# Kernel optimization log

Measured on AMD Instinct MI355X. Metric: run time of the kernel, lower is better.

## Reference

```python
import jax, jax.numpy as jnp
import numpy as np

EPS = 1e-5

def _bn(h, g, b):
    # BatchNorm1d with batch statistics (biased variance), eps=1e-5
    m = jnp.mean(h, axis=0)
    v = jnp.var(h, axis=0)
    return (h - m) * jax.lax.rsqrt(v + EPS) * g + b

def setup_inputs() -> dict:
    key = jax.random.key(0)
    ks = jax.random.split(key, 12)
    N, E, F = 100000, 500000, 128
    D = 2 * F  # 256
    s = 1.0 / np.sqrt(D)
    inp = {
        "x": jax.random.normal(ks[0], (N, F), dtype=jnp.float32),
        "edge_index": jax.random.randint(ks[1], (2, E), 0, N, dtype=jnp.int64),
        "W4": jax.random.normal(ks[2], (D, D), jnp.float32) * s,
        "b4": jnp.zeros((D,), jnp.float32),
        "g4": jnp.ones((D,), jnp.float32),
        "be4": jnp.zeros((D,), jnp.float32),
        "W1": jax.random.normal(ks[3], (D, D), jnp.float32) * s,
        "b1": jnp.zeros((D,), jnp.float32),
        "g1": jnp.ones((D,), jnp.float32),
        "be1": jnp.zeros((D,), jnp.float32),
        "W2": jax.random.normal(ks[4], (D, D), jnp.float32) * s,
        "b2": jnp.zeros((D,), jnp.float32),
        "g2": jnp.ones((D,), jnp.float32),
        "be2": jnp.zeros((D,), jnp.float32),
        "Wf": jax.random.normal(ks[5], (D, 1), jnp.float32) * s,
        "bf": jnp.zeros((1,), jnp.float32),
    }
    return inp

def reference(x, edge_index, W4, b4, g4, be4, W1, b1, g1, be1, W2, b2, g2, be2, Wf, bf):
    # gather + concat: [E, 2*F]
    edge_x = jnp.concatenate((x[edge_index[0]], x[edge_index[1]]), axis=1)
    # block 4: Linear -> BN -> ReLU (dropout = identity in eval)
    edge_x = jax.nn.relu(_bn(edge_x @ W4 + b4, g4, be4))
    # block 1 with residual
    out1 = jax.nn.relu(_bn(edge_x @ W1 + b1, g1, be1)) + edge_x
    # block 2 with residual
    out2 = jax.nn.relu(_bn(out1 @ W2 + b2, g2, be2)) + out1
    # final projection -> flatten to [E]
    return jnp.ravel(out2 @ Wf + bf)
```

## Files before the change

kernel.cpp:

```cpp
#include <hip/hip_runtime.h>
#include <hip/hip_bf16.h>
#include <stdint.h>


typedef __attribute__((ext_vector_type(8))) short short8;
typedef __attribute__((ext_vector_type(4))) float f32x4;

__device__ __forceinline__ unsigned short bf16b(float f) {
  unsigned int u = __float_as_uint(f);
  return (unsigned short)((u + 0x7fffu + ((u >> 16) & 1u)) >> 16);
}
__device__ __forceinline__ unsigned int packbf(float lo, float hi) {
  return (unsigned int)bf16b(lo) | ((unsigned int)bf16b(hi) << 16);
}
__device__ __forceinline__ float bflo(unsigned int u) { return __uint_as_float(u << 16); }
__device__ __forceinline__ float bfhi(unsigned int u) { return __uint_as_float(u & 0xffff0000u); }
__device__ __forceinline__ float bfs(short s) { return __uint_as_float(((unsigned int)(unsigned short)s) << 16); }
__device__ __forceinline__ float relu_(float x) { return fmaxf(x, 0.0f); }

__global__ __launch_bounds__(256) void k_init(const int* __restrict__ ei,
                                              float* __restrict__ stats, int* __restrict__ flag) {
  const int t = threadIdx.x;
  for (int i = t; i < 12288; i += 256) stats[i] = 0.f;
  if (t == 0) {
    int o = 0;
#pragma unroll
    for (int i = 0; i < 32; ++i) o |= ei[2 * i + 1];
    *flag = (o == 0) ? 1 : 0;
  }
}

__global__ __launch_bounds__(256) void k_bail(float* __restrict__ out, const float* __restrict__ bfp, int E) {
  const int i = blockIdx.x * 256 + threadIdx.x;
  if (i < E) out[i] = bfp[0];
}

__global__ __launch_bounds__(256) void k_prep(
    const float* __restrict__ W4, const float* __restrict__ W1, const float* __restrict__ W2,
    unsigned short* __restrict__ wt4, unsigned short* __restrict__ wt1, unsigned short* __restrict__ wt2)
{
  const int b = blockIdx.x;
  const int t = threadIdx.x;
  const int wi = b >> 6;
  const int r = b & 63;
  const float* W = (wi == 0) ? W4 : (wi == 1) ? W1 : W2;
  unsigned short* Wt = (wi == 0) ? wt4 : (wi == 1) ? wt1 : wt2;
  const int flat = r * 1024 + t * 4;
  const int n = flat >> 8;
  const int k = flat & 255;
  ushort4 o;
  o.x = bf16b(W[(k + 0) * 256 + n]);
  o.y = bf16b(W[(k + 1) * 256 + n]);
  o.z = bf16b(W[(k + 2) * 256 + n]);
  o.w = bf16b(W[(k + 3) * 256 + n]);
  *(ushort4*)(Wt + flat) = o;
}

__global__ __launch_bounds__(256) void k_stats(
    const float* __restrict__ stats, const float* __restrict__ g, const float* __restrict__ be,
    const float* __restrict__ bias, float* __restrict__ scale, float invE)
{
  const int c = threadIdx.x;
  float s = 0.f, q = 0.f;
#pragma unroll
  for (int sl = 0; sl < 8; ++sl) { s += stats[sl * 512 + c]; q += stats[sl * 512 + 256 + c]; }
  const float mean = s * invE;
  const float var = q * invE - mean * mean;
  const float a = g[c] * rsqrtf(var + 1e-5f);
  const float cstd = be[c] - mean * a;
  scale[c] = a;
  scale[256 + c] = cstd;
  scale[512 + c] = fmaf(a, bias[c], cstd);
}

template<int MODE>
__global__ __attribute__((amdgpu_waves_per_eu(2, 2))) __launch_bounds__(512) void kp(
    const void* Asrc, const int* __restrict__ ei, const int* __restrict__ flagp,
    const unsigned short* __restrict__ Wt, const float* __restrict__ bias,
    const float* __restrict__ scst, const float* __restrict__ scep, const float* __restrict__ wf,
    unsigned short* __restrict__ buf, float* __restrict__ stats, float* __restrict__ out,
    const float* __restrict__ bfp, int E, int MT)
{
  __shared__ __align__(16) char lds[131072];
  float* sRed = (float*)(lds + 65536);

  const int t = threadIdx.x;
  const int b = blockIdx.x;
  const int per = MT >> 8, rem = MT & 255;
  const int t0 = b * per + (b < rem ? b : rem);
  const int t1 = t0 + per + (b < rem ? 1 : 0);

  const int l = t & 63, wv = t >> 6;
  const int sw = (l & 7) << 4;
  const int subc = t & 31;
  const int lrq = (l >> 4) << 2;
  const int kq = (l >> 4) << 4;
  const int flag = (MODE == 1) ? flagp[0] : 0;
  const float bf0 = (MODE == 3) ? bfp[0] : 0.f;

  float bj[2] = {0.f, 0.f};
  if (MODE == 1 || MODE == 2 || MODE == 4) {
    bj[0] = bias[wv * 32 + (l & 15)];
    bj[1] = bias[wv * 32 + 16 + (l & 15)];
  }
  float aE[2], cE[2], wE[2];
  if (MODE == 3 || MODE == 5) {
#pragma unroll
    for (int j = 0; j < 2; ++j) {
      const int c = wv * 32 + j * 16 + (l & 15);
      aE[j] = scep[c]; cE[j] = scep[512 + c]; wE[j] = wf[c];
    }
  }
  float4 aa0, aa1, cc0, cc1;
  if (MODE == 2 || MODE == 3) {
    aa0 = *(const float4*)(scst + subc * 8);
    aa1 = *(const float4*)(scst + subc * 8 + 4);
    cc0 = *(const float4*)(scst + 512 + subc * 8);
    cc1 = *(const float4*)(scst + 512 + subc * 8 + 4);
  }
  float ssum[2] = {0.f, 0.f}, ssq[2] = {0.f, 0.f};

  uint4 pf[4];
#define PREFETCH(TT)                                                            \
  if (MODE == 1) {                                                              \
    const float* xf = (const float*)Asrc;                                       \
    _Pragma("unroll")                                                           \
    for (int r = 0; r < 4; ++r) {                                               \
      const int c = t + r * 512;                                                \
      const int row = c >> 5;                                                   \
      int e = (TT) * 64 + row; if (e >= E) e = E - 1;                           \
      const int idx = (subc < 16) ? e : (E + e);                                \
      const int node = flag ? ei[2 * idx] : ei[idx];                            \
      const float* s = xf + node * 128 + (subc & 15) * 8;                       \
      float4 f0 = *(const float4*)s;                                            \
      float4 f1 = *(const float4*)(s + 4);                                      \
      pf[r].x = packbf(f0.x, f0.y); pf[r].y = packbf(f0.z, f0.w);               \
      pf[r].z = packbf(f1.x, f1.y); pf[r].w = packbf(f1.z, f1.w);               \
    }                                                                           \
  } else {                                                                      \
    const uint4* s = (const uint4*)((const char*)Asrc + (size_t)(TT) * 32768);  \
    _Pragma("unroll")                                                           \
    for (int r = 0; r < 4; ++r) pf[r] = s[t + r * 512];                         \
  }

#define STAGE_A(AP)                                                             \
  _Pragma("unroll")                                                             \
  for (int r = 0; r < 4; ++r) {                                                 \
    const int c = t + r * 512;                                                  \
    const int row = c >> 5;                                                     \
    uint4 v = pf[r];                                                            \
    if (MODE == 2 || MODE == 3) {                                               \
      unsigned int* vp = (unsigned int*)&v;                                     \
      vp[0] = packbf(relu_(fmaf(bflo(vp[0]), aa0.x, cc0.x)),                    \
                     relu_(fmaf(bfhi(vp[0]), aa0.y, cc0.y)));                   \
      vp[1] = packbf(relu_(fmaf(bflo(vp[1]), aa0.z, cc0.z)),                    \
                     relu_(fmaf(bfhi(vp[1]), aa0.w, cc0.w)));                   \
      vp[2] = packbf(relu_(fmaf(bflo(vp[2]), aa1.x, cc1.x)),                    \
                     relu_(fmaf(bfhi(vp[2]), aa1.y, cc1.y)));                   \
      vp[3] = packbf(relu_(fmaf(bflo(vp[3]), aa1.z, cc1.z)),                    \
                     relu_(fmaf(bfhi(vp[3]), aa1.w, cc1.w)));                   \
    }                                                                           \
    *(uint4*)((AP) + row * 512 + ((subc * 16) ^ ((row & 7) << 4))) = v;         \
  }

  PREFETCH(t0);
#pragma unroll
  for (int r = 0; r < 16; ++r) {
    const int c = t + r * 512;
    uint4 v = *(const uint4*)(Wt + c * 8);
    const int n = c >> 5;
    *(uint4*)(lds + n * 512 + (((c & 31) * 16) ^ ((n & 7) << 4))) = v;
  }
  __syncthreads();
  short8 bf8[8][2];
#pragma unroll
  for (int s8 = 0; s8 < 8; ++s8) {
    const int kb = (s8 * 64 + kq) ^ sw;
#pragma unroll
    for (int j = 0; j < 2; ++j) {
      const int bn = wv * 32 + j * 16 + (l & 15);
      bf8[s8][j] = *(const short8*)(lds + bn * 512 + kb);
    }
  }
  __syncthreads();
  char* aT0 = lds;
  char* aT1 = lds + 32768;

  STAGE_A(aT0);
  if (t0 + 1 < t1) PREFETCH(t0 + 1);
  __syncthreads();

  int cur = 0;
  for (int tt = t0; tt < t1; ++tt) {
    char* aC = cur ? aT1 : aT0;
    char* aN = cur ? aT0 : aT1;
    if (tt + 1 < t1) {
      STAGE_A(aN);
      if (tt + 2 < t1) PREFETCH(tt + 2);
    }

    f32x4 acc[4][2];
    f32x4 zz = {0.f, 0.f, 0.f, 0.f};
#pragma unroll
    for (int i = 0; i < 4; ++i) { acc[i][0] = zz; acc[i][1] = zz; }
#pragma unroll
    for (int s8 = 0; s8 < 8; ++s8) {
      const int kb = (s8 * 64 + kq) ^ sw;
#pragma unroll
      for (int i = 0; i < 4; ++i) {
        short8 a = *(const short8*)(aC + (i * 16 + (l & 15)) * 512 + kb);
        acc[i][0] = __builtin_amdgcn_mfma_f32_16x16x32_bf16(a, bf8[s8][0], acc[i][0], 0, 0, 0);
        acc[i][1] = __builtin_amdgcn_mfma_f32_16x16x32_bf16(a, bf8[s8][1], acc[i][1], 0, 0, 0);
      }
    }

    if (MODE == 1 || MODE == 2 || MODE == 4) {
#pragma unroll
      for (int i = 0; i < 4; ++i) {
        const int r0 = tt * 64 + i * 16 + lrq;
#pragma unroll
        for (int j = 0; j < 2; ++j)
#pragma unroll
          for (int q = 0; q < 4; ++q) {
            const float v = acc[i][j][q] + bj[j];
            if (r0 + q < E) { ssum[j] += v; ssq[j] = fmaf(v, v, ssq[j]); }
          }
      }
    }
    if (MODE == 3 || MODE == 5) {
#pragma unroll
      for (int i = 0; i < 4; ++i) {
#pragma unroll
        for (int q = 0; q < 4; ++q) {
          const int lrow = i * 16 + lrq + q;
          float p = 0.f;
#pragma unroll
          for (int j = 0; j < 2; ++j) {
            float v = relu_(fmaf(acc[i][j][q], aE[j], cE[j]));
            if (MODE == 3) {
              const int col = wv * 32 + j * 16 + (l & 15);
              v += bfs(*(const short*)(aC + lrow * 512 + ((col * 2) ^ ((lrow & 7) << 4))));
              acc[i][j][q] = v;
            }
            p = fmaf(v, wE[j], p);
          }
          p += __shfl_xor(p, 1); p += __shfl_xor(p, 2);
          p += __shfl_xor(p, 4); p += __shfl_xor(p, 8);
          if ((l & 15) == 0) sRed[lrow * 8 + wv] = p;
        }
      }
    }
    __syncthreads();

    if (MODE == 1 || MODE == 3) {
      const int odd = l & 1;
#pragma unroll
      for (int i = 0; i < 4; ++i) {
        const int r0 = i * 16 + lrq;
#pragma unroll
        for (int j = 0; j < 2; ++j) {
          float v0 = acc[i][j][0], v1 = acc[i][j][1], v2 = acc[i][j][2], v3 = acc[i][j][3];
          float p0 = __shfl_xor(v0, 1), p1 = __shfl_xor(v1, 1);
          float p2 = __shfl_xor(v2, 1), p3 = __shfl_xor(v3, 1);
          float loA = odd ? p2 : v0, hiA = odd ? v2 : p0;
          float loB = odd ? p3 : v1, hiB = odd ? v3 : p1;
          const int ra = r0 + (odd ? 2 : 0);
          const int cp2 = ((wv * 32 + j * 16 + (l & 15)) & ~1) * 2;
          *(unsigned int*)(aC + (ra + 0) * 512 + (cp2 ^ (((ra + 0) & 7) << 4))) = packbf(loA, hiA);
          *(unsigned int*)(aC + (ra + 1) * 512 + (cp2 ^ (((ra + 1) & 7) << 4))) = packbf(loB, hiB);
        }
      }
      if (MODE == 3 && t < 64) {
        const int row = tt * 64 + t;
        if (row < E) {
          float s = 0.f;
#pragma unroll
          for (int w = 0; w < 8; ++w) s += sRed[t * 8 + w];
          out[row] = s + bf0;
        }
      }
      __syncthreads();
      char* d = (char*)buf + (size_t)tt * 32768;
#pragma unroll
      for (int r = 0; r < 4; ++r) {
        const int c = t + r * 512;
        const int row = c >> 5;
        uint4 v = *(const uint4*)(aC + row * 512 + (((c & 31) * 16) ^ ((row & 7) << 4)));
        *(uint4*)(d + c * 16) = v;
      }
      __syncthreads();
    } else if (MODE == 5) {
      if (t < 64) {
        const int row = tt * 64 + t;
        if (row < E) {
          float s = 0.f;
#pragma unroll
          for (int w = 0; w < 8; ++w) s += sRed[t * 8 + w];
          out[row] += s;
        }
      }
      __syncthreads();
    }
    cur ^= 1;
  }

  if (MODE == 1 || MODE == 2 || MODE == 4) {
#pragma unroll
    for (int j = 0; j < 2; ++j) {
      ssum[j] += __shfl_xor(ssum[j], 16); ssum[j] += __shfl_xor(ssum[j], 32);
      ssq[j]  += __shfl_xor(ssq[j], 16);  ssq[j]  += __shfl_xor(ssq[j], 32);
    }
    if (l < 16) {
      sRed[wv * 32 + l] = ssum[0];
      sRed[wv * 32 + 16 + l] = ssum[1];
      sRed[256 + wv * 32 + l] = ssq[0];
      sRed[256 + wv * 32 + 16 + l] = ssq[1];
    }
    __syncthreads();
    if (t < 512) atomicAdd(&stats[(b & 7) * 512 + t], sRed[t]);
  }
#undef PREFETCH
#undef STAGE_A
}

extern "C" void kernel_launch(void* const* d_in, const int* in_sizes, int n_in,
                              void* d_out, int out_size, void* d_ws, size_t ws_size,
                              hipStream_t stream) {
  const float* x   = (const float*)d_in[0];
  const int*   ei  = (const int*)d_in[1];
  const float* W4  = (const float*)d_in[2];
  const float* b4  = (const float*)d_in[3];
  const float* g4  = (const float*)d_in[4];
  const float* be4 = (const float*)d_in[5];
  const float* W1  = (const float*)d_in[6];
  const float* b1  = (const float*)d_in[7];
  const float* g1  = (const float*)d_in[8];
  const float* be1 = (const float*)d_in[9];
  const float* W2  = (const float*)d_in[10];
  const float* b2  = (const float*)d_in[11];
  const float* g2  = (const float*)d_in[12];
  const float* be2 = (const float*)d_in[13];
  const float* Wf  = (const float*)d_in[14];
  const float* bfp = (const float*)d_in[15];
  float* out = (float*)d_out;

  const int E = out_size;
  const int MT = (E + 63) / 64;
  const float invE = 1.0f / (float)E;

  char* ws = (char*)d_ws;
  unsigned short* wt4 = (unsigned short*)(ws);
  unsigned short* wt1 = (unsigned short*)(ws + 131072);
  unsigned short* wt2 = (unsigned short*)(ws + 262144);
  float* stats = (float*)(ws + 393216);
  float* scale = (float*)(ws + 442368);
  int*   flag  = (int*)(ws + 451584);
  const size_t fixed = 458752;
  const size_t bufbytes = (size_t)MT * 32768;
  unsigned short* buf = (unsigned short*)(ws + fixed);

  if (ws_size < fixed + bufbytes) {
    k_bail<<<(E + 255) / 256, 256, 0, stream>>>(out, bfp, E);
    return;
  }

  k_init<<<1, 256, 0, stream>>>(ei, stats, flag);
  k_prep<<<192, 256, 0, stream>>>(W4, W1, W2, wt4, wt1, wt2);

  kp<1><<<256, 512, 0, stream>>>((const void*)x, ei, flag, wt4, b4,
                                 nullptr, nullptr, nullptr, buf, stats, nullptr, bfp, E, MT);
  k_stats<<<1, 256, 0, stream>>>(stats, g4, be4, b4, scale, invE);
  kp<2><<<256, 512, 0, stream>>>((const void*)buf, nullptr, flag, wt1, b1,
                                 scale, nullptr, nullptr, nullptr, stats + 4096, nullptr, bfp, E, MT);
  k_stats<<<1, 256, 0, stream>>>(stats + 4096, g1, be1, b1, scale + 768, invE);
  kp<3><<<256, 512, 0, stream>>>((const void*)buf, nullptr, flag, wt1, nullptr,
                                 scale, scale + 768, Wf, buf, nullptr, out, bfp, E, MT);
  kp<4><<<256, 512, 0, stream>>>((const void*)buf, nullptr, flag, wt2, b2,
                                 nullptr, nullptr, nullptr, nullptr, stats + 8192, nullptr, bfp, E, MT);
  k_stats<<<1, 256, 0, stream>>>(stats + 8192, g2, be2, b2, scale + 1536, invE);
  kp<5><<<256, 512, 0, stream>>>((const void*)buf, nullptr, flag, wt2, nullptr,
                                 nullptr, scale + 1536, Wf, nullptr, nullptr, out, bfp, E, MT);
}
```

Measured before the change: 678.8 us.

## Double per-CU occupancy: halve LDS, load weight fragments from global, 512 blocks

Raises the kernel's waves-per-EU target from 2 to 4 and shrinks the shared buffer from 128 KB to 64 KB plus a small separate reduction array, so two 512-thread blocks can share a CU. The launch grid grows from 256 to 512 blocks, with tile partitioning made parametric in the block count. Weight fragments now go straight from global memory into registers instead of being staged through LDS, which drops two barriers and an LDS round trip per block. The tighter per-thread register budget risks spills, since the 16 short8 weight fragments and the accumulators are held in registers throughout.

Measured after the change: 1.342 ms. 97.7% more time.

```diff
diff --git a/kernel.cpp b/kernel.cpp
--- a/kernel.cpp
+++ b/kernel.cpp
@@ -74,19 +74,19 @@
 }
 
 template<int MODE>
-__global__ __attribute__((amdgpu_waves_per_eu(2, 2))) __launch_bounds__(512) void kp(
+__global__ __attribute__((amdgpu_waves_per_eu(4, 4))) __launch_bounds__(512) void kp(
     const void* Asrc, const int* __restrict__ ei, const int* __restrict__ flagp,
     const unsigned short* __restrict__ Wt, const float* __restrict__ bias,
     const float* __restrict__ scst, const float* __restrict__ scep, const float* __restrict__ wf,
     unsigned short* __restrict__ buf, float* __restrict__ stats, float* __restrict__ out,
-    const float* __restrict__ bfp, int E, int MT)
+    const float* __restrict__ bfp, int E, int MT, int NBLK)
 {
-  __shared__ __align__(16) char lds[131072];
-  float* sRed = (float*)(lds + 65536);
+  __shared__ __align__(16) char lds[65536];
+  __shared__ float sRed[512];
 
   const int t = threadIdx.x;
   const int b = blockIdx.x;
-  const int per = MT >> 8, rem = MT & 255;
+  const int per = MT / NBLK, rem = MT % NBLK;
   const int t0 = b * per + (b < rem ? b : rem);
   const int t1 = t0 + per + (b < rem ? 1 : 0);
 
@@ -164,25 +164,16 @@
   }
 
   PREFETCH(t0);
-#pragma unroll
-  for (int r = 0; r < 16; ++r) {
-    const int c = t + r * 512;
-    uint4 v = *(const uint4*)(Wt + c * 8);
-    const int n = c >> 5;
-    *(uint4*)(lds + n * 512 + (((c & 31) * 16) ^ ((n & 7) << 4))) = v;
-  }
-  __syncthreads();
   short8 bf8[8][2];
-#pragma unroll
-  for (int s8 = 0; s8 < 8; ++s8) {
-    const int kb = (s8 * 64 + kq) ^ sw;
-#pragma unroll
-    for (int j = 0; j < 2; ++j) {
-      const int bn = wv * 32 + j * 16 + (l & 15);
-      bf8[s8][j] = *(const short8*)(lds + bn * 512 + kb);
-    }
-  }
-  __syncthreads();
+  {
+    const unsigned short* wp = Wt + (unsigned)(l & 15) * 256 + ((l >> 4) << 3);
+#pragma unroll
+    for (int s8 = 0; s8 < 8; ++s8)
+#pragma unroll
+      for (int j = 0; j < 2; ++j)
+        bf8[s8][j] = *(const short8*)(wp + (wv * 32 + j * 16) * 256 + s8 * 32);
+  }
+
   char* aT0 = lds;
   char* aT1 = lds + 32768;
 
@@ -346,6 +337,7 @@
 
   const int E = out_size;
   const int MT = (E + 63) / 64;
+  const int NBLK = 512;
   const float invE = 1.0f / (float)E;
 
   char* ws = (char*)d_ws;
@@ -367,17 +359,17 @@
   k_init<<<1, 256, 0, stream>>>(ei, stats, flag);
   k_prep<<<192, 256, 0, stream>>>(W4, W1, W2, wt4, wt1, wt2);
 
-  kp<1><<<256, 512, 0, stream>>>((const void*)x, ei, flag, wt4, b4,
-                                 nullptr, nullptr, nullptr, buf, stats, nullptr, bfp, E, MT);
+  kp<1><<<NBLK, 512, 0, stream>>>((const void*)x, ei, flag, wt4, b4,
+                                  nullptr, nullptr, nullptr, buf, stats, nullptr, bfp, E, MT, NBLK);
   k_stats<<<1, 256, 0, stream>>>(stats, g4, be4, b4, scale, invE);
-  kp<2><<<256, 512, 0, stream>>>((const void*)buf, nullptr, flag, wt1, b1,
-                                 scale, nullptr, nullptr, nullptr, stats + 4096, nullptr, bfp, E, MT);
+  kp<2><<<NBLK, 512, 0, stream>>>((const void*)buf, nullptr, flag, wt1, b1,
+                                  scale, nullptr, nullptr, nullptr, stats + 4096, nullptr, bfp, E, MT, NBLK);
   k_stats<<<1, 256, 0, stream>>>(stats + 4096, g1, be1, b1, scale + 768, invE);
-  kp<3><<<256, 512, 0, stream>>>((const void*)buf, nullptr, flag, wt1, nullptr,
-                                 scale, scale + 768, Wf, buf, nullptr, out, bfp, E, MT);
-  kp<4><<<256, 512, 0, stream>>>((const void*)buf, nullptr, flag, wt2, b2,
-                                 nullptr, nullptr, nullptr, nullptr, stats + 8192, nullptr, bfp, E, MT);
+  kp<3><<<NBLK, 512, 0, stream>>>((const void*)buf, nullptr, flag, wt1, nullptr,
+                                  scale, scale + 768, Wf, buf, nullptr, out, bfp, E, MT, NBLK);
+  kp<4><<<NBLK, 512, 0, stream>>>((const void*)buf, nullptr, flag, wt2, b2,
+                                  nullptr, nullptr, nullptr, nullptr, stats + 8192, nullptr, bfp, E, MT, NBLK);
   k_stats<<<1, 256, 0, stream>>>(stats + 8192, g2, be2, b2, scale + 1536, invE);
-  kp<5><<<256, 512, 0, stream>>>((const void*)buf, nullptr, flag, wt2, nullptr,
-                                 nullptr, scale + 1536, Wf, nullptr, nullptr, out, bfp, E, MT);
-}
+  kp<5><<<NBLK, 512, 0, stream>>>((const void*)buf, nullptr, flag, wt2, nullptr,
+                                  nullptr, scale + 1536, Wf, nullptr, nullptr, out, bfp, E, MT, NBLK);
+}
```
